# Performance work log

Hardware: AMD Instinct MI355X
Metric: run time of the kernel (lower is better)

Reference implementation:

```python
import jax, jax.numpy as jnp
import numpy as np

EPS = 1e-5

def setup_inputs() -> dict:
    key = jax.random.key(0)
    ks = jax.random.split(key, 8)
    B, C, H, W = 16, 512, 41, 41
    N = H * W
    Ck = C // 2
    return {
        "x": jax.random.normal(ks[0], (B, C, H, W), jnp.float32),
        "fg_sim": jax.random.uniform(ks[1], (B, N, N), jnp.float32),
        "bg_sim": jax.random.uniform(ks[2], (B, N, N), jnp.float32),
        "Wq": jax.random.normal(ks[3], (Ck, C), jnp.float32) * 0.02,
        "bq": jax.random.normal(ks[4], (Ck,), jnp.float32) * 0.02,
        "Wk": jax.random.normal(ks[5], (Ck, C), jnp.float32) * 0.02,
        "bk": jax.random.normal(ks[6], (Ck,), jnp.float32) * 0.02,
        "gamma": jax.random.normal(ks[7], (1,), jnp.float32) * 0.1,
    }

def reference(x, fg_sim, bg_sim, Wq, bq, Wk, bk, gamma):
    B, C, H, W = x.shape
    N = H * W
    Ck = Wk.shape[0]
    xf = x.reshape(B, C, N)                       # [B, C, N]
    # 1x1 convs = channel matmuls
    query = jnp.einsum('kc,bcn->bnk', Wq, xf) + bq  # [B, N, Ck]
    key_ = jnp.einsum('kc,bcn->bkn', Wk, xf) + bk[None, :, None]  # [B, Ck, N]
    sim = jnp.einsum('bnk,bkm->bnm', query, key_) * (Ck ** -0.5)  # [B, N, N]
    sim = sim * fg_sim
    # masked_normalize: min-subtract, mask, sum-normalize
    min_v = jnp.min(sim, axis=-1, keepdims=True)
    x1 = (sim - min_v) * fg_sim
    sim = x1 / (jnp.sum(x1, axis=-1, keepdims=True) + EPS)
    sim = sim + bg_sim
    value = xf.transpose(0, 2, 1)                 # [B, N, C]
    context = jnp.einsum('bnm,bmc->bnc', sim, value)  # [B, N, C]
    context = context.transpose(0, 2, 1).reshape(B, C, H, W)
    fuse = gamma[0] * context + x
    return fuse
```

## Files before the change

kernel.cpp:

```cpp
#include <hip/hip_runtime.h>
#include <math.h>

#define B_   16
#define C_   512
#define N_   1681
#define Np   1792
#define CK_  256
#define EPSV 1e-5f
#define SCALE 0.0625f

typedef __bf16 bf16x8 __attribute__((ext_vector_type(8)));
typedef __bf16 bf16x4 __attribute__((ext_vector_type(4)));
typedef float  f32x4  __attribute__((ext_vector_type(4)));

__device__ __forceinline__
void stage_tile(const char* gbase, int ld_bytes, char* lds, int w, int lane)
{
    #pragma unroll
    for (int i = 0; i < 4; ++i) {
        int chunk = (i * 4 + w) * 64 + lane;
        int row   = chunk >> 3;
        int col   = chunk & 7;
        int scol  = col ^ (row & 7);
        const char* g = gbase + (size_t)row * ld_bytes + scol * 16;
        char* l = lds + (size_t)(i * 4 + w) * 1024;
        __builtin_amdgcn_global_load_lds(
            (const __attribute__((address_space(1))) void*)g,
            (__attribute__((address_space(3))) void*)l, 16, 0, 0);
    }
}

__device__ __forceinline__
void mma_tile(const __bf16* As, const __bf16* Bs, f32x4 acc[4][4], int wr, int wc, int lane)
{
    const int l15 = lane & 15, quad = lane >> 4;
    #pragma unroll
    for (int kk = 0; kk < 2; ++kk) {
        bf16x8 af[4], bfr[4];
        #pragma unroll
        for (int i = 0; i < 4; ++i) {
            int row = wr * 64 + i * 16 + l15;
            int c   = (kk * 4 + quad) ^ (row & 7);
            af[i] = *(const bf16x8*)(As + row * 64 + c * 8);
        }
        #pragma unroll
        for (int j = 0; j < 4; ++j) {
            int row = wc * 64 + j * 16 + l15;
            int c   = (kk * 4 + quad) ^ (row & 7);
            bfr[j] = *(const bf16x8*)(Bs + row * 64 + c * 8);
        }
        #pragma unroll
        for (int i = 0; i < 4; ++i)
            #pragma unroll
            for (int j = 0; j < 4; ++j)
                acc[i][j] = __builtin_amdgcn_mfma_f32_16x16x32_bf16(
                    af[i], bfr[j], acc[i][j], 0, 0, 0);
    }
}

__global__ __launch_bounds__(256)
void cvt_w_kernel(const float* __restrict__ Wq, const float* __restrict__ Wk,
                  const float* __restrict__ bq, const float* __restrict__ bk,
                  __bf16* __restrict__ Wh, float* __restrict__ b2)
{
    int idx = blockIdx.x * 1024 + threadIdx.x * 4;
    #pragma unroll
    for (int p = 0; p < 4; ++p) {
        int e = idx + p;
        int row = e >> 9, col = e & 511;
        float v = (row < 256) ? Wq[row * 512 + col] : Wk[(row - 256) * 512 + col];
        Wh[e] = (__bf16)v;
    }
    if (blockIdx.x == 0) {
        int t = threadIdx.x;
        b2[t]       = bq[t];
        b2[256 + t] = bk[t];
    }
}

__global__ __launch_bounds__(256)
void cvt_x_kernel(const float* __restrict__ x,
                  __bf16* __restrict__ xh, __bf16* __restrict__ xt)
{
    __shared__ float tile[32][33];
    const int t = threadIdx.x;
    const int n0 = blockIdx.x * 32, c0 = blockIdx.y * 32, b = blockIdx.z;
    const float* xb = x + (size_t)b * C_ * N_;
    #pragma unroll
    for (int p = 0; p < 4; ++p) {
        int lin = p * 256 + t;
        int i = lin >> 5, j = lin & 31;
        int n = n0 + j;
        float v = (n < N_) ? xb[(size_t)(c0 + i) * N_ + n] : 0.0f;
        tile[i][j] = v;
        xh[(size_t)b * C_ * Np + (size_t)(c0 + i) * Np + n] = (__bf16)v;
    }
    __syncthreads();
    #pragma unroll
    for (int p = 0; p < 4; ++p) {
        int lin = p * 256 + t;
        int i = lin >> 5, j = lin & 31;
        xt[(size_t)b * Np * C_ + (size_t)(n0 + i) * C_ + (c0 + j)] = (__bf16)tile[j][i];
    }
}

__global__ __launch_bounds__(256)
void proj_kernel(const __bf16* __restrict__ xt, const __bf16* __restrict__ Wh,
                 const float* __restrict__ b2, __bf16* __restrict__ QKt)
{
    __shared__ __bf16 As[128 * 64];
    __shared__ __bf16 Bs[128 * 64];
    const int t = threadIdx.x, w = t >> 6, lane = t & 63;
    const int n0 = blockIdx.x * 128, k20 = blockIdx.y * 128, b = blockIdx.z;
    const char* Abase = (const char*)xt + ((size_t)b * Np + n0) * (C_ * 2);
    const char* Bbase = (const char*)Wh + (size_t)k20 * (C_ * 2);

    f32x4 acc[4][4] = {};
    for (int k0 = 0; k0 < C_; k0 += 64) {
        stage_tile(Abase + k0 * 2, C_ * 2, (char*)As, w, lane);
        stage_tile(Bbase + k0 * 2, C_ * 2, (char*)Bs, w, lane);
        __syncthreads();
        mma_tile(As, Bs, acc, w >> 1, w & 1, lane);
        __syncthreads();
    }
    const int l15 = lane & 15, quad = lane >> 4;
    __bf16* ob = QKt + (size_t)b * Np * 512;
    #pragma unroll
    for (int j = 0; j < 4; ++j) {
        int k2 = k20 + (w & 1) * 64 + j * 16 + l15;
        float bias = b2[k2];
        #pragma unroll
        for (int i = 0; i < 4; ++i)
            #pragma unroll
            for (int r = 0; r < 4; ++r) {
                int n = n0 + (w >> 1) * 64 + i * 16 + quad * 4 + r;
                ob[(size_t)n * 512 + k2] = (__bf16)(acc[i][j][r] + bias);
            }
    }
}

__global__ __launch_bounds__(256)
void sim_kernel(const __bf16* __restrict__ QKt, __bf16* __restrict__ S)
{
    __shared__ __bf16 As[128 * 64];
    __shared__ __bf16 Bs[128 * 64];
    const int t = threadIdx.x, w = t >> 6, lane = t & 63;
    const int m0 = blockIdx.x * 128, n0 = blockIdx.y * 128, b = blockIdx.z;
    const char* base = (const char*)QKt + (size_t)b * Np * 1024;
    const char* Abase = base + (size_t)n0 * 1024;
    const char* Bbase = base + (size_t)m0 * 1024 + 512;

    f32x4 acc[4][4] = {};
    for (int k0 = 0; k0 < CK_; k0 += 64) {
        stage_tile(Abase + k0 * 2, 1024, (char*)As, w, lane);
        stage_tile(Bbase + k0 * 2, 1024, (char*)Bs, w, lane);
        __syncthreads();
        mma_tile(As, Bs, acc, w >> 1, w & 1, lane);
        __syncthreads();
    }
    const int l15 = lane & 15, quad = lane >> 4;
    __bf16* Sb = S + (size_t)b * Np * Np;
    #pragma unroll
    for (int i = 0; i < 4; ++i)
        #pragma unroll
        for (int r = 0; r < 4; ++r) {
            int n = n0 + (w >> 1) * 64 + i * 16 + quad * 4 + r;
            #pragma unroll
            for (int j = 0; j < 4; ++j) {
                int m = m0 + (w & 1) * 64 + j * 16 + l15;
                Sb[(size_t)n * Np + m] = (__bf16)(acc[i][j][r] * SCALE);
            }
        }
}

__global__ __launch_bounds__(256, 4)
void norm_kernel(const float* __restrict__ fg, const float* __restrict__ bg,
                 __bf16* __restrict__ S)
{
    const int t = threadIdx.x;
    const int wid = t >> 6, lane = t & 63;
    const int n = blockIdx.x * 4 + wid;
    const int b = blockIdx.y;
    if (n >= N_) return;

    __bf16* Srow = S + (size_t)b * Np * Np + (size_t)n * Np;
    const float* fgrow = fg + ((size_t)b * N_ + n) * N_;
    const float* bgrow = bg + ((size_t)b * N_ + n) * N_;

    float sv[7][4];
    float fv[7][4];
    float lmin = INFINITY, aSum = 0.0f, fSum = 0.0f;

    #pragma unroll
    for (int i = 0; i < 7; ++i) {
        const int m0 = i * 256 + lane * 4;
        bf16x4 sr = *(const bf16x4*)(Srow + m0);
        f32x4 f;
        if (m0 + 4 <= N_) {
            f = *(const f32x4*)(fgrow + m0);
        } else {
            f[0] = (m0 + 0 < N_) ? fgrow[m0 + 0] : 0.0f;
            f[1] = (m0 + 1 < N_) ? fgrow[m0 + 1] : 0.0f;
            f[2] = (m0 + 2 < N_) ? fgrow[m0 + 2] : 0.0f;
            f[3] = (m0 + 3 < N_) ? fgrow[m0 + 3] : 0.0f;
        }
        #pragma unroll
        for (int k = 0; k < 4; ++k) {
            const bool valid = (m0 + k) < N_;
            const float fk = f[k];
            const float svk = (float)sr[k] * fk;
            sv[i][k] = svk;
            fv[i][k] = fk;
            aSum += svk * fk;
            fSum += fk;
            lmin = fminf(lmin, valid ? svk : INFINITY);
        }
    }

    #pragma unroll
    for (int off = 1; off < 64; off <<= 1) {
        lmin = fminf(lmin, __shfl_xor(lmin, off, 64));
        aSum += __shfl_xor(aSum, off, 64);
        fSum += __shfl_xor(fSum, off, 64);
    }
    const float inv = 1.0f / ((aSum - lmin * fSum) + EPSV);

    #pragma unroll
    for (int i = 0; i < 7; ++i) {
        const int m0 = i * 256 + lane * 4;
        f32x4 g;
        if (m0 + 4 <= N_) {
            g = *(const f32x4*)(bgrow + m0);
        } else {
            g[0] = (m0 + 0 < N_) ? bgrow[m0 + 0] : 0.0f;
            g[1] = (m0 + 1 < N_) ? bgrow[m0 + 1] : 0.0f;
            g[2] = (m0 + 2 < N_) ? bgrow[m0 + 2] : 0.0f;
            g[3] = (m0 + 3 < N_) ? bgrow[m0 + 3] : 0.0f;
        }
        bf16x4 o;
        #pragma unroll
        for (int k = 0; k < 4; ++k) {
            const bool valid = (m0 + k) < N_;
            const float x1 = (sv[i][k] - lmin) * fv[i][k];
            o[k] = (__bf16)(valid ? (x1 * inv + g[k]) : 0.0f);
        }
        *(bf16x4*)(Srow + m0) = o;
    }
}

__global__ __launch_bounds__(256)
void ctx_kernel(const __bf16* __restrict__ xh, const __bf16* __restrict__ Ap,
                const float* __restrict__ x, const float* __restrict__ gamma,
                float* __restrict__ out)
{
    __shared__ __bf16 As[128 * 64];
    __shared__ __bf16 Bs[128 * 64];
    const int t = threadIdx.x, w = t >> 6, lane = t & 63;
    const int c0 = blockIdx.x * 128, n0 = blockIdx.y * 128, b = blockIdx.z;
    const char* Abase = (const char*)xh + ((size_t)b * C_ + c0) * (Np * 2);
    const char* Bbase = (const char*)Ap + ((size_t)b * Np + n0) * (Np * 2);

    f32x4 acc[4][4] = {};
    for (int k0 = 0; k0 < Np; k0 += 64) {
        stage_tile(Abase + k0 * 2, Np * 2, (char*)As, w, lane);
        stage_tile(Bbase + k0 * 2, Np * 2, (char*)Bs, w, lane);
        __syncthreads();
        mma_tile(As, Bs, acc, w >> 1, w & 1, lane);
        __syncthreads();
    }
    const int l15 = lane & 15, quad = lane >> 4;
    const float g = gamma[0];
    const float* xb = x + (size_t)b * C_ * N_;
    float* ob = out + (size_t)b * C_ * N_;
    #pragma unroll
    for (int i = 0; i < 4; ++i)
        #pragma unroll
        for (int r = 0; r < 4; ++r) {
            int c = c0 + (w >> 1) * 64 + i * 16 + quad * 4 + r;
            #pragma unroll
            for (int j = 0; j < 4; ++j) {
                int n = n0 + (w & 1) * 64 + j * 16 + l15;
                if (n < N_) {
                    size_t idx = (size_t)c * N_ + n;
                    ob[idx] = g * acc[i][j][r] + xb[idx];
                }
            }
        }
}

extern "C" void kernel_launch(void* const* d_in, const int* in_sizes, int n_in,
                              void* d_out, int out_size, void* d_ws, size_t ws_size,
                              hipStream_t stream)
{
    const float* x     = (const float*)d_in[0];
    const float* fg    = (const float*)d_in[1];
    const float* bg    = (const float*)d_in[2];
    const float* Wq    = (const float*)d_in[3];
    const float* bq    = (const float*)d_in[4];
    const float* Wk    = (const float*)d_in[5];
    const float* bk    = (const float*)d_in[6];
    const float* gamma = (const float*)d_in[7];
    float* out = (float*)d_out;

    char* p = (char*)d_ws;
    __bf16* xh  = (__bf16*)p; p += (size_t)B_ * C_ * Np * 2;
    __bf16* xt  = (__bf16*)p; p += (size_t)B_ * Np * C_ * 2;
    __bf16* QKt = (__bf16*)p; p += (size_t)B_ * Np * 512 * 2;
    __bf16* S   = (__bf16*)p; p += (size_t)B_ * Np * Np * 2;
    __bf16* Wh  = (__bf16*)p; p += (size_t)512 * 512 * 2;
    float*  b2  = (float*)p;

    cvt_w_kernel<<<dim3(256), dim3(256), 0, stream>>>(Wq, Wk, bq, bk, Wh, b2);
    cvt_x_kernel<<<dim3(Np / 32, C_ / 32, B_), dim3(256), 0, stream>>>(x, xh, xt);
    proj_kernel<<<dim3(Np / 128, 4, B_), dim3(256), 0, stream>>>(xt, Wh, b2, QKt);
    sim_kernel<<<dim3(Np / 128, Np / 128, B_), dim3(256), 0, stream>>>(QKt, S);
    norm_kernel<<<dim3((N_ + 3) / 4, B_), dim3(256), 0, stream>>>(fg, bg, S);
    ctx_kernel<<<dim3(C_ / 128, Np / 128, B_), dim3(256), 0, stream>>>(xh, S, x, gamma, out);
}
```

Before: 662.1 us.

## Double-buffer LDS in GEMM kernels and swizzle block order across XCDs

Replaces the single-buffered load/sync/compute loop in the proj, sim and ctx GEMMs with a two-stage LDS ping-pong. The next K tile is issued via global_load_lds while MFMAs run on the current one, with one barrier per iteration. Launches are flattened to 1D grids, and block IDs are remapped so consecutive tiles sharing the same batch operands land on the same XCD for L2 reuse. This doubles LDS use per block (64 KB), which may lower occupancy.

```diff
diff --git a/kernel.cpp b/kernel.cpp
--- a/kernel.cpp
+++ b/kernel.cpp
@@ -12,6 +12,11 @@
 typedef __bf16 bf16x8 __attribute__((ext_vector_type(8)));
 typedef __bf16 bf16x4 __attribute__((ext_vector_type(4)));
 typedef float  f32x4  __attribute__((ext_vector_type(4)));
+
+__device__ __forceinline__ int xcd_swz(int orig, int q)
+{
+    return (orig & 7) * q + (orig >> 3);
+}
 
 __device__ __forceinline__
 void stage_tile(const char* gbase, int ld_bytes, char* lds, int w, int lane)
@@ -58,6 +63,27 @@
     }
 }
 
+#define PIPELINED_GEMM(Abase, lda, Bbase, ldb, NT)                              \
+    stage_tile(Abase, lda, (char*)As[0], w, lane);                              \
+    stage_tile(Bbase, ldb, (char*)Bs[0], w, lane);                              \
+    asm volatile("s_waitcnt vmcnt(0)" ::: "memory");                            \
+    __builtin_amdgcn_s_barrier();                                               \
+    {                                                                           \
+        int cur = 0;                                                            \
+        for (int kt = 0; kt < (NT); ++kt) {                                     \
+            if (kt + 1 < (NT)) {                                                \
+                stage_tile((Abase) + (kt + 1) * 128, lda, (char*)As[cur ^ 1], w, lane); \
+                stage_tile((Bbase) + (kt + 1) * 128, ldb, (char*)Bs[cur ^ 1], w, lane); \
+            }                                                                   \
+            mma_tile(As[cur], Bs[cur], acc, w >> 1, w & 1, lane);               \
+            if (kt + 1 < (NT)) {                                                \
+                asm volatile("s_waitcnt vmcnt(0)" ::: "memory");                \
+                __builtin_amdgcn_s_barrier();                                   \
+            }                                                                   \
+            cur ^= 1;                                                           \
+        }                                                                       \
+    }
+
 __global__ __launch_bounds__(256)
 void cvt_w_kernel(const float* __restrict__ Wq, const float* __restrict__ Wk,
                   const float* __restrict__ bq, const float* __restrict__ bk,
@@ -108,21 +134,19 @@
 void proj_kernel(const __bf16* __restrict__ xt, const __bf16* __restrict__ Wh,
                  const float* __restrict__ b2, __bf16* __restrict__ QKt)
 {
-    __shared__ __bf16 As[128 * 64];
-    __shared__ __bf16 Bs[128 * 64];
+    __shared__ __bf16 As[2][128 * 64];
+    __shared__ __bf16 Bs[2][128 * 64];
     const int t = threadIdx.x, w = t >> 6, lane = t & 63;
-    const int n0 = blockIdx.x * 128, k20 = blockIdx.y * 128, b = blockIdx.z;
+    const int wg = xcd_swz(blockIdx.x, 112);
+    const int k20 = (wg & 3) * 128;
+    const int n0  = ((wg >> 2) % 14) * 128;
+    const int b   = wg / 56;
     const char* Abase = (const char*)xt + ((size_t)b * Np + n0) * (C_ * 2);
     const char* Bbase = (const char*)Wh + (size_t)k20 * (C_ * 2);
 
     f32x4 acc[4][4] = {};
-    for (int k0 = 0; k0 < C_; k0 += 64) {
-        stage_tile(Abase + k0 * 2, C_ * 2, (char*)As, w, lane);
-        stage_tile(Bbase + k0 * 2, C_ * 2, (char*)Bs, w, lane);
-        __syncthreads();
-        mma_tile(As, Bs, acc, w >> 1, w & 1, lane);
-        __syncthreads();
-    }
+    PIPELINED_GEMM(Abase, C_ * 2, Bbase, C_ * 2, C_ / 64)
+
     const int l15 = lane & 15, quad = lane >> 4;
     __bf16* ob = QKt + (size_t)b * Np * 512;
     #pragma unroll
@@ -142,22 +166,20 @@
 __global__ __launch_bounds__(256)
 void sim_kernel(const __bf16* __restrict__ QKt, __bf16* __restrict__ S)
 {
-    __shared__ __bf16 As[128 * 64];
-    __shared__ __bf16 Bs[128 * 64];
+    __shared__ __bf16 As[2][128 * 64];
+    __shared__ __bf16 Bs[2][128 * 64];
     const int t = threadIdx.x, w = t >> 6, lane = t & 63;
-    const int m0 = blockIdx.x * 128, n0 = blockIdx.y * 128, b = blockIdx.z;
+    const int wg = xcd_swz(blockIdx.x, 392);
+    const int m0 = (wg % 14) * 128;
+    const int n0 = ((wg / 14) % 14) * 128;
+    const int b  = wg / 196;
     const char* base = (const char*)QKt + (size_t)b * Np * 1024;
     const char* Abase = base + (size_t)n0 * 1024;
     const char* Bbase = base + (size_t)m0 * 1024 + 512;
 
     f32x4 acc[4][4] = {};
-    for (int k0 = 0; k0 < CK_; k0 += 64) {
-        stage_tile(Abase + k0 * 2, 1024, (char*)As, w, lane);
-        stage_tile(Bbase + k0 * 2, 1024, (char*)Bs, w, lane);
-        __syncthreads();
-        mma_tile(As, Bs, acc, w >> 1, w & 1, lane);
-        __syncthreads();
-    }
+    PIPELINED_GEMM(Abase, 1024, Bbase, 1024, CK_ / 64)
+
     const int l15 = lane & 15, quad = lane >> 4;
     __bf16* Sb = S + (size_t)b * Np * Np;
     #pragma unroll
@@ -253,21 +275,19 @@
                 const float* __restrict__ x, const float* __restrict__ gamma,
                 float* __restrict__ out)
 {
-    __shared__ __bf16 As[128 * 64];
-    __shared__ __bf16 Bs[128 * 64];
+    __shared__ __bf16 As[2][128 * 64];
+    __shared__ __bf16 Bs[2][128 * 64];
     const int t = threadIdx.x, w = t >> 6, lane = t & 63;
-    const int c0 = blockIdx.x * 128, n0 = blockIdx.y * 128, b = blockIdx.z;
+    const int wg = xcd_swz(blockIdx.x, 112);
+    const int c0 = (wg & 3) * 128;
+    const int n0 = ((wg >> 2) % 14) * 128;
+    const int b  = wg / 56;
     const char* Abase = (const char*)xh + ((size_t)b * C_ + c0) * (Np * 2);
     const char* Bbase = (const char*)Ap + ((size_t)b * Np + n0) * (Np * 2);
 
     f32x4 acc[4][4] = {};
-    for (int k0 = 0; k0 < Np; k0 += 64) {
-        stage_tile(Abase + k0 * 2, Np * 2, (char*)As, w, lane);
-        stage_tile(Bbase + k0 * 2, Np * 2, (char*)Bs, w, lane);
-        __syncthreads();
-        mma_tile(As, Bs, acc, w >> 1, w & 1, lane);
-        __syncthreads();
-    }
+    PIPELINED_GEMM(Abase, Np * 2, Bbase, Np * 2, Np / 64)
+
     const int l15 = lane & 15, quad = lane >> 4;
     const float g = gamma[0];
     const float* xb = x + (size_t)b * C_ * N_;
@@ -312,8 +332,8 @@
 
     cvt_w_kernel<<<dim3(256), dim3(256), 0, stream>>>(Wq, Wk, bq, bk, Wh, b2);
     cvt_x_kernel<<<dim3(Np / 32, C_ / 32, B_), dim3(256), 0, stream>>>(x, xh, xt);
-    proj_kernel<<<dim3(Np / 128, 4, B_), dim3(256), 0, stream>>>(xt, Wh, b2, QKt);
-    sim_kernel<<<dim3(Np / 128, Np / 128, B_), dim3(256), 0, stream>>>(QKt, S);
+    proj_kernel<<<dim3(896), dim3(256), 0, stream>>>(xt, Wh, b2, QKt);
+    sim_kernel<<<dim3(3136), dim3(256), 0, stream>>>(QKt, S);
     norm_kernel<<<dim3((N_ + 3) / 4, B_), dim3(256), 0, stream>>>(fg, bg, S);
-    ctx_kernel<<<dim3(C_ / 128, Np / 128, B_), dim3(256), 0, stream>>>(xh, S, x, gamma, out);
-}
+    ctx_kernel<<<dim3(896), dim3(256), 0, stream>>>(xh, S, x, gamma, out);
+}
```

New measurement: 672.8 us. No clear change (+1.6%).

## Rewrite GEMM kernels with 256x256 tiles, 4-slot LDS pipeline and XCD swizzle

Applied to the files above, without the earlier changes.

Replaces the simple 128x128 single-buffered GEMM loop in proj, sim and ctx with a shared 256x256-tile, 512-thread core. It uses a 4-slot, 128KB dynamic LDS ring that prefetches two K-steps ahead, with split A/B staging interleaved between MFMA batches and s_setprio around them. Block indices are remapped so neighbouring tiles land on the same XCD for L2 reuse. This aims to hide global-load latency and raise arithmetic intensity. The cost is higher register and LDS pressure and more tile padding waste on the 1792-padded dimensions.

```diff
diff --git a/kernel.cpp b/kernel.cpp
--- a/kernel.cpp
+++ b/kernel.cpp
@@ -9,52 +9,97 @@
 #define EPSV 1e-5f
 #define SCALE 0.0625f
 
+#define SLOT_BYTES 32768
+#define LDS_BYTES  131072
+
 typedef __bf16 bf16x8 __attribute__((ext_vector_type(8)));
 typedef __bf16 bf16x4 __attribute__((ext_vector_type(4)));
 typedef float  f32x4  __attribute__((ext_vector_type(4)));
 
+__device__ __forceinline__ int xcd_swz(int orig, int q)
+{
+    return (orig & 7) * q + (orig >> 3);
+}
+
 __device__ __forceinline__
-void stage_tile(const char* gbase, int ld_bytes, char* lds, int w, int lane)
-{
-    #pragma unroll
-    for (int i = 0; i < 4; ++i) {
-        int chunk = (i * 4 + w) * 64 + lane;
-        int row   = chunk >> 3;
-        int col   = chunk & 7;
-        int scol  = col ^ (row & 7);
-        const char* g = gbase + (size_t)row * ld_bytes + scol * 16;
-        char* l = lds + (size_t)(i * 4 + w) * 1024;
+void stage_half(const char* g, int ld_bytes, char* l, int tid)
+{
+    #pragma unroll
+    for (int r = 0; r < 2; ++r) {
+        int chunk = r * 512 + tid;
+        int row   = chunk >> 2;
+        int col   = chunk & 3;
+        int scol  = col ^ ((row >> 1) & 3);
         __builtin_amdgcn_global_load_lds(
-            (const __attribute__((address_space(1))) void*)g,
-            (__attribute__((address_space(3))) void*)l, 16, 0, 0);
+            (const __attribute__((address_space(1))) void*)(g + (size_t)row * ld_bytes + scol * 16),
+            (__attribute__((address_space(3))) void*)(l + (size_t)chunk * 16), 16, 0, 0);
     }
 }
 
 __device__ __forceinline__
-void mma_tile(const __bf16* As, const __bf16* Bs, f32x4 acc[4][4], int wr, int wc, int lane)
-{
+bf16x8 lds_frag(const __bf16* base, int row, int quad)
+{
+    int c = quad ^ ((row >> 1) & 3);
+    return *(const bf16x8*)(base + (size_t)row * 32 + c * 8);
+}
+
+__device__ __forceinline__
+void gemm_core(const char* __restrict__ Ab, int lda,
+               const char* __restrict__ Bb, int ldb,
+               char* slots, f32x4 acc[8][4], int nt)
+{
+    const int tid = threadIdx.x;
+    const int wid = tid >> 6, lane = tid & 63;
+    const int wm = wid >> 2, wn = wid & 3;
     const int l15 = lane & 15, quad = lane >> 4;
-    #pragma unroll
-    for (int kk = 0; kk < 2; ++kk) {
+
+    stage_half(Ab,      lda, slots,                           tid);
+    stage_half(Bb,      ldb, slots + 16384,                   tid);
+    stage_half(Ab + 64, lda, slots + SLOT_BYTES,              tid);
+    stage_half(Bb + 64, ldb, slots + SLOT_BYTES + 16384,      tid);
+    asm volatile("s_waitcnt vmcnt(4)" ::: "memory");
+    __builtin_amdgcn_s_barrier();
+
+    for (int t = 0; t < nt; ++t) {
+        const __bf16* As = (const __bf16*)(slots + (size_t)(t & 3) * SLOT_BYTES);
+        const __bf16* Bs = (const __bf16*)(slots + (size_t)(t & 3) * SLOT_BYTES + 16384);
+        char* dst = slots + (size_t)((t + 2) & 3) * SLOT_BYTES;
+        const bool more = (t + 2) < nt;
+
         bf16x8 af[4], bfr[4];
         #pragma unroll
-        for (int i = 0; i < 4; ++i) {
-            int row = wr * 64 + i * 16 + l15;
-            int c   = (kk * 4 + quad) ^ (row & 7);
-            af[i] = *(const bf16x8*)(As + row * 64 + c * 8);
-        }
-        #pragma unroll
-        for (int j = 0; j < 4; ++j) {
-            int row = wc * 64 + j * 16 + l15;
-            int c   = (kk * 4 + quad) ^ (row & 7);
-            bfr[j] = *(const bf16x8*)(Bs + row * 64 + c * 8);
-        }
+        for (int i = 0; i < 4; ++i)
+            af[i] = lds_frag(As, wm * 128 + i * 16 + l15, quad);
+        #pragma unroll
+        for (int j = 0; j < 4; ++j)
+            bfr[j] = lds_frag(Bs, wn * 64 + j * 16 + l15, quad);
+        if (more) stage_half(Ab + (size_t)(t + 2) * 64, lda, dst, tid);
+        __builtin_amdgcn_s_setprio(1);
         #pragma unroll
         for (int i = 0; i < 4; ++i)
             #pragma unroll
             for (int j = 0; j < 4; ++j)
                 acc[i][j] = __builtin_amdgcn_mfma_f32_16x16x32_bf16(
                     af[i], bfr[j], acc[i][j], 0, 0, 0);
+        __builtin_amdgcn_s_setprio(0);
+        __builtin_amdgcn_s_barrier();
+
+        #pragma unroll
+        for (int i = 0; i < 4; ++i)
+            af[i] = lds_frag(As, wm * 128 + (4 + i) * 16 + l15, quad);
+        if (more) stage_half(Bb + (size_t)(t + 2) * 64, ldb, dst + 16384, tid);
+        __builtin_amdgcn_s_setprio(1);
+        #pragma unroll
+        for (int i = 0; i < 4; ++i)
+            #pragma unroll
+            for (int j = 0; j < 4; ++j)
+                acc[4 + i][j] = __builtin_amdgcn_mfma_f32_16x16x32_bf16(
+                    af[i], bfr[j], acc[4 + i][j], 0, 0, 0);
+        __builtin_amdgcn_s_setprio(0);
+
+        if (more) asm volatile("s_waitcnt vmcnt(4)" ::: "memory");
+        else      asm volatile("s_waitcnt vmcnt(0)" ::: "memory");
+        __builtin_amdgcn_s_barrier();
     }
 }
 
@@ -104,70 +149,66 @@
     }
 }
 
-__global__ __launch_bounds__(256)
+__global__ __launch_bounds__(512, 2)
 void proj_kernel(const __bf16* __restrict__ xt, const __bf16* __restrict__ Wh,
                  const float* __restrict__ b2, __bf16* __restrict__ QKt)
 {
-    __shared__ __bf16 As[128 * 64];
-    __shared__ __bf16 Bs[128 * 64];
-    const int t = threadIdx.x, w = t >> 6, lane = t & 63;
-    const int n0 = blockIdx.x * 128, k20 = blockIdx.y * 128, b = blockIdx.z;
+    extern __shared__ char slots[];
+    const int wg = xcd_swz(blockIdx.x, 28);
+    const int k20 = (wg & 1) * 256;
+    const int n0  = ((wg >> 1) % 7) * 256;
+    const int b   = wg / 14;
     const char* Abase = (const char*)xt + ((size_t)b * Np + n0) * (C_ * 2);
     const char* Bbase = (const char*)Wh + (size_t)k20 * (C_ * 2);
 
-    f32x4 acc[4][4] = {};
-    for (int k0 = 0; k0 < C_; k0 += 64) {
-        stage_tile(Abase + k0 * 2, C_ * 2, (char*)As, w, lane);
-        stage_tile(Bbase + k0 * 2, C_ * 2, (char*)Bs, w, lane);
-        __syncthreads();
-        mma_tile(As, Bs, acc, w >> 1, w & 1, lane);
-        __syncthreads();
-    }
+    f32x4 acc[8][4] = {};
+    gemm_core(Abase, C_ * 2, Bbase, C_ * 2, slots, acc, C_ / 32);
+
+    const int tid = threadIdx.x, wid = tid >> 6, lane = tid & 63;
+    const int wm = wid >> 2, wn = wid & 3;
     const int l15 = lane & 15, quad = lane >> 4;
     __bf16* ob = QKt + (size_t)b * Np * 512;
     #pragma unroll
     for (int j = 0; j < 4; ++j) {
-        int k2 = k20 + (w & 1) * 64 + j * 16 + l15;
+        int k2 = k20 + wn * 64 + j * 16 + l15;
         float bias = b2[k2];
         #pragma unroll
-        for (int i = 0; i < 4; ++i)
+        for (int i = 0; i < 8; ++i)
             #pragma unroll
             for (int r = 0; r < 4; ++r) {
-                int n = n0 + (w >> 1) * 64 + i * 16 + quad * 4 + r;
+                int n = n0 + wm * 128 + i * 16 + quad * 4 + r;
                 ob[(size_t)n * 512 + k2] = (__bf16)(acc[i][j][r] + bias);
             }
     }
 }
 
-__global__ __launch_bounds__(256)
+__global__ __launch_bounds__(512, 2)
 void sim_kernel(const __bf16* __restrict__ QKt, __bf16* __restrict__ S)
 {
-    __shared__ __bf16 As[128 * 64];
-    __shared__ __bf16 Bs[128 * 64];
-    const int t = threadIdx.x, w = t >> 6, lane = t & 63;
-    const int m0 = blockIdx.x * 128, n0 = blockIdx.y * 128, b = blockIdx.z;
+    extern __shared__ char slots[];
+    const int wg = xcd_swz(blockIdx.x, 98);
+    const int m0 = (wg % 7) * 256;
+    const int n0 = ((wg / 7) % 7) * 256;
+    const int b  = wg / 49;
     const char* base = (const char*)QKt + (size_t)b * Np * 1024;
     const char* Abase = base + (size_t)n0 * 1024;
     const char* Bbase = base + (size_t)m0 * 1024 + 512;
 
-    f32x4 acc[4][4] = {};
-    for (int k0 = 0; k0 < CK_; k0 += 64) {
-        stage_tile(Abase + k0 * 2, 1024, (char*)As, w, lane);
-        stage_tile(Bbase + k0 * 2, 1024, (char*)Bs, w, lane);
-        __syncthreads();
-        mma_tile(As, Bs, acc, w >> 1, w & 1, lane);
-        __syncthreads();
-    }
+    f32x4 acc[8][4] = {};
+    gemm_core(Abase, 1024, Bbase, 1024, slots, acc, CK_ / 32);
+
+    const int tid = threadIdx.x, wid = tid >> 6, lane = tid & 63;
+    const int wm = wid >> 2, wn = wid & 3;
     const int l15 = lane & 15, quad = lane >> 4;
     __bf16* Sb = S + (size_t)b * Np * Np;
     #pragma unroll
-    for (int i = 0; i < 4; ++i)
+    for (int i = 0; i < 8; ++i)
         #pragma unroll
         for (int r = 0; r < 4; ++r) {
-            int n = n0 + (w >> 1) * 64 + i * 16 + quad * 4 + r;
+            int n = n0 + wm * 128 + i * 16 + quad * 4 + r;
             #pragma unroll
             for (int j = 0; j < 4; ++j) {
-                int m = m0 + (w & 1) * 64 + j * 16 + l15;
+                int m = m0 + wn * 64 + j * 16 + l15;
                 Sb[(size_t)n * Np + m] = (__bf16)(acc[i][j][r] * SCALE);
             }
         }
@@ -248,38 +289,36 @@
     }
 }
 
-__global__ __launch_bounds__(256)
+__global__ __launch_bounds__(512, 2)
 void ctx_kernel(const __bf16* __restrict__ xh, const __bf16* __restrict__ Ap,
                 const float* __restrict__ x, const float* __restrict__ gamma,
                 float* __restrict__ out)
 {
-    __shared__ __bf16 As[128 * 64];
-    __shared__ __bf16 Bs[128 * 64];
-    const int t = threadIdx.x, w = t >> 6, lane = t & 63;
-    const int c0 = blockIdx.x * 128, n0 = blockIdx.y * 128, b = blockIdx.z;
+    extern __shared__ char slots[];
+    const int wg = xcd_swz(blockIdx.x, 28);
+    const int c0 = (wg & 1) * 256;
+    const int n0 = ((wg >> 1) % 7) * 256;
+    const int b  = wg / 14;
     const char* Abase = (const char*)xh + ((size_t)b * C_ + c0) * (Np * 2);
     const char* Bbase = (const char*)Ap + ((size_t)b * Np + n0) * (Np * 2);
 
-    f32x4 acc[4][4] = {};
-    for (int k0 = 0; k0 < Np; k0 += 64) {
-        stage_tile(Abase + k0 * 2, Np * 2, (char*)As, w, lane);
-        stage_tile(Bbase + k0 * 2, Np * 2, (char*)Bs, w, lane);
-        __syncthreads();
-        mma_tile(As, Bs, acc, w >> 1, w & 1, lane);
-        __syncthreads();
-    }
+    f32x4 acc[8][4] = {};
+    gemm_core(Abase, Np * 2, Bbase, Np * 2, slots, acc, Np / 32);
+
+    const int tid = threadIdx.x, wid = tid >> 6, lane = tid & 63;
+    const int wm = wid >> 2, wn = wid & 3;
     const int l15 = lane & 15, quad = lane >> 4;
     const float g = gamma[0];
     const float* xb = x + (size_t)b * C_ * N_;
     float* ob = out + (size_t)b * C_ * N_;
     #pragma unroll
-    for (int i = 0; i < 4; ++i)
+    for (int i = 0; i < 8; ++i)
         #pragma unroll
         for (int r = 0; r < 4; ++r) {
-            int c = c0 + (w >> 1) * 64 + i * 16 + quad * 4 + r;
+            int c = c0 + wm * 128 + i * 16 + quad * 4 + r;
             #pragma unroll
             for (int j = 0; j < 4; ++j) {
-                int n = n0 + (w & 1) * 64 + j * 16 + l15;
+                int n = n0 + wn * 64 + j * 16 + l15;
                 if (n < N_) {
                     size_t idx = (size_t)c * N_ + n;
                     ob[idx] = g * acc[i][j][r] + xb[idx];
@@ -310,10 +349,21 @@
     __bf16* Wh  = (__bf16*)p; p += (size_t)512 * 512 * 2;
     float*  b2  = (float*)p;
 
+    static bool attr_done = false;
+    if (!attr_done) {
+        hipFuncSetAttribute((const void*)proj_kernel,
+                            hipFuncAttributeMaxDynamicSharedMemorySize, LDS_BYTES);
+        hipFuncSetAttribute((const void*)sim_kernel,
+                            hipFuncAttributeMaxDynamicSharedMemorySize, LDS_BYTES);
+        hipFuncSetAttribute((const void*)ctx_kernel,
+                            hipFuncAttributeMaxDynamicSharedMemorySize, LDS_BYTES);
+        attr_done = true;
+    }
+
     cvt_w_kernel<<<dim3(256), dim3(256), 0, stream>>>(Wq, Wk, bq, bk, Wh, b2);
     cvt_x_kernel<<<dim3(Np / 32, C_ / 32, B_), dim3(256), 0, stream>>>(x, xh, xt);
-    proj_kernel<<<dim3(Np / 128, 4, B_), dim3(256), 0, stream>>>(xt, Wh, b2, QKt);
-    sim_kernel<<<dim3(Np / 128, Np / 128, B_), dim3(256), 0, stream>>>(QKt, S);
+    proj_kernel<<<dim3(224), dim3(512), LDS_BYTES, stream>>>(xt, Wh, b2, QKt);
+    sim_kernel<<<dim3(784), dim3(512), LDS_BYTES, stream>>>(QKt, S);
     norm_kernel<<<dim3((N_ + 3) / 4, B_), dim3(256), 0, stream>>>(fg, bg, S);
-    ctx_kernel<<<dim3(C_ / 128, Np / 128, B_), dim3(256), 0, stream>>>(xh, S, x, gamma, out);
-}
+    ctx_kernel<<<dim3(224), dim3(512), LDS_BYTES, stream>>>(xh, S, x, gamma, out);
+}
```

New measurement: 626.2 us. -5.4%, faster.
